# Kernel optimization log

Hardware: AMD Instinct MI355X
Metric: run time of the kernel (lower is better)

## Reference

```python
import jax, jax.numpy as jnp
import numpy as np

# dims: M=512 new tokens, N=2048 model dim, D=128 head dim, H=16 heads,
# L=4096 cache length, P=2048 cache write offset

def setup_inputs() -> dict:
    key = jax.random.key(0)
    k0, k1, k2, k3 = jax.random.split(key, 4)
    M, N, D, L = 512, 2048, 128, 4096
    X = jax.random.normal(k0, (M, N), jnp.float32)
    # scale weights ~1/sqrt(N) so projections have unit-ish scale
    W_qkv = jax.random.normal(k1, (N, 3 * N), jnp.float32) * (N ** -0.5)
    H = N // D
    cache_K = jax.random.normal(k2, (H, L, D), jnp.float32)
    # realistic cache state: keys stored in cache are RMS-normalized
    cache_K = cache_K * jax.lax.rsqrt(jnp.mean(cache_K * cache_K, axis=-1, keepdims=True))
    cache_V = jax.random.normal(k3, (H, L, D), jnp.float32)
    return {"X": X, "W_qkv": W_qkv, "cache_K": cache_K, "cache_V": cache_V, "P": 2048}


def reference(X, W_qkv, cache_K, cache_V, P):
    M = X.shape[0]
    H, L, D = cache_K.shape
    qkv = X @ W_qkv                              # [M, 3N]
    q, k, v = jnp.split(qkv, 3, axis=-1)         # each [M, N]
    q = q.reshape(M, H, D).transpose(1, 0, 2)    # [H, M, D]
    k = k.reshape(M, H, D).transpose(1, 0, 2)
    v = v.reshape(M, H, D).transpose(1, 0, 2)
    # RMS-style normalization (no learned gain, no eps in original)
    q = q * jax.lax.rsqrt(jnp.mean(q * q, axis=-1, keepdims=True))
    k = k * jax.lax.rsqrt(jnp.mean(k * k, axis=-1, keepdims=True))
    # scatter-update into KV cache at position P
    Kc = jax.lax.dynamic_update_slice(cache_K, k, (0, P, 0))  # [H, L, D]
    Vc = jax.lax.dynamic_update_slice(cache_V, v, (0, P, 0))
    # unmasked, unscaled attention over the full cache (faithful to original:
    # plain exp/sum, no max-subtraction, no 1/sqrt(D))
    scores = jnp.einsum('hmd,hld->hml', q, Kc)   # [H, M, L]
    w = jnp.exp(scores)
    w = w / jnp.sum(w, axis=-1, keepdims=True)
    out = jnp.einsum('hml,hld->hmd', w, Vc)      # [H, M, D]
    return out.transpose(1, 0, 2).reshape(M, H * D)
```

## Files before the change

kernel.cpp:

```cpp
#include <hip/hip_runtime.h>
#include <math.h>

typedef _Float16 half_t;
typedef _Float16 half8 __attribute__((ext_vector_type(8)));
typedef _Float16 half4_t __attribute__((ext_vector_type(4)));
typedef _Float16 half2_t __attribute__((ext_vector_type(2)));
typedef float floatx4 __attribute__((ext_vector_type(4)));

#define M_TOK 512
#define N_DIM 2048
#define D_HEAD 128
#define H_HEADS 16
#define L_CACHE 4096
#define THREE_N 6144
#define NCHUNK 8
#define LCHUNK 512

__global__ __launch_bounds__(256) void prep_kernel(const float* __restrict__ W,
                                                   const float* __restrict__ X,
                                                   half_t* __restrict__ W16T,
                                                   half_t* __restrict__ X16) {
    __shared__ half_t tile[64 * 66];
    int b = blockIdx.x;
    int t = threadIdx.x;

    if (b < 3072) {
        int n0 = (b % 96) * 64, k0 = (b / 96) * 64;
        {
            int k = t >> 2, c0 = (t & 3) * 16;
            const float* src = W + (size_t)(k0 + k) * THREE_N + n0 + c0;
            float4 v[4];
#pragma unroll
            for (int j = 0; j < 4; ++j) v[j] = *(const float4*)(src + j * 4);
#pragma unroll
            for (int j = 0; j < 4; ++j) {
                tile[(c0 + j * 4 + 0) * 66 + k] = (half_t)v[j].x;
                tile[(c0 + j * 4 + 1) * 66 + k] = (half_t)v[j].y;
                tile[(c0 + j * 4 + 2) * 66 + k] = (half_t)v[j].z;
                tile[(c0 + j * 4 + 3) * 66 + k] = (half_t)v[j].w;
            }
        }
        __syncthreads();
        {
            int n = t >> 2, kg = (t & 3) * 16;
            half_t* dst = W16T + (size_t)(n0 + n) * N_DIM + k0 + kg;
            *(half8*)(dst) = *(half8*)&tile[n * 66 + kg];
            *(half8*)(dst + 8) = *(half8*)&tile[n * 66 + kg + 8];
        }
        return;
    }
    b -= 3072;
    {
        size_t i = (size_t)b * 2048 + t * 4;
        float4 v0 = *(const float4*)(X + i);
        float4 v1 = *(const float4*)(X + i + 1024);
        half4_t h0 = {(half_t)v0.x, (half_t)v0.y, (half_t)v0.z, (half_t)v0.w};
        half4_t h1 = {(half_t)v1.x, (half_t)v1.y, (half_t)v1.z, (half_t)v1.w};
        *(half4_t*)(X16 + i) = h0;
        *(half4_t*)(X16 + i + 1024) = h1;
    }
}

__global__ __launch_bounds__(256, 5) void mega_kernel(const half_t* __restrict__ X16,
                                                      const half_t* __restrict__ W16T,
                                                      const float* __restrict__ cK,
                                                      const float* __restrict__ cV,
                                                      const int* __restrict__ Pp,
                                                      half_t* __restrict__ Q16,
                                                      half_t* __restrict__ K16,
                                                      half_t* __restrict__ V16T) {
    __shared__ __align__(16) char smem[25088];
    const int t = threadIdx.x;
    int b = blockIdx.x;

    if (b >= 384) {
        b -= 384;
        const int P = *Pp;
        if (b < 1024) {
            int h = b >> 6, l0 = (b & 63) * 64;
            if (l0 >= P && l0 + 64 <= P + M_TOK) return;
            size_t base = ((size_t)h * L_CACHE + l0) * D_HEAD;
            float4 v[8];
#pragma unroll
            for (int i = 0; i < 8; ++i)
                v[i] = *(const float4*)(cK + base + i * 1024 + t * 4);
#pragma unroll
            for (int i = 0; i < 8; ++i) {
                int row = l0 + ((i * 1024 + t * 4) >> 7);
                half4_t hh = {(half_t)v[i].x, (half_t)v[i].y, (half_t)v[i].z, (half_t)v[i].w};
                if (row < P || row >= P + M_TOK)
                    *(half4_t*)(K16 + base + i * 1024 + t * 4) = hh;
            }
            return;
        }
        b -= 1024;
        {
            int h = b >> 7;
            int rem = b & 127;
            int lt = rem >> 1, dt = rem & 1;
            int l0 = lt * 64, d0 = dt * 64;
            if (l0 >= P && l0 + 64 <= P + M_TOK) return;
            bool overlap = (l0 < P + M_TOK) && (l0 + 64 > P);
            half_t* tile = (half_t*)smem;
            {
                int l = t >> 2, c0 = (t & 3) * 16;
                const float* src = cV + ((size_t)h * L_CACHE + l0 + l) * D_HEAD + d0 + c0;
                float4 v[4];
#pragma unroll
                for (int j = 0; j < 4; ++j) v[j] = *(const float4*)(src + j * 4);
#pragma unroll
                for (int j = 0; j < 4; ++j) {
                    tile[(c0 + j * 4 + 0) * 66 + l] = (half_t)v[j].x;
                    tile[(c0 + j * 4 + 1) * 66 + l] = (half_t)v[j].y;
                    tile[(c0 + j * 4 + 2) * 66 + l] = (half_t)v[j].z;
                    tile[(c0 + j * 4 + 3) * 66 + l] = (half_t)v[j].w;
                }
            }
            __syncthreads();
            {
                int d = t >> 2, lg = (t & 3) * 16;
                half_t* dst = V16T + ((size_t)h * D_HEAD + d0 + d) * L_CACHE + l0 + lg;
                if (!overlap) {
                    *(half8*)(dst) = *(half8*)&tile[d * 66 + lg];
                    *(half8*)(dst + 8) = *(half8*)&tile[d * 66 + lg + 8];
                } else {
#pragma unroll
                    for (int j = 0; j < 16; ++j) {
                        int l = l0 + lg + j;
                        if (l < P || l >= P + M_TOK) dst[j] = tile[d * 66 + lg + j];
                    }
                }
            }
            return;
        }
    }

    half_t* As = (half_t*)smem;
    half_t* Bs = (half_t*)(smem + 8192);
    half_t* Vt = (half_t*)smem;
    float* ssb = (float*)(smem + 24576);
    const int wid = t >> 6, lane = t & 63;
    const int quad = lane >> 4, ln = lane & 15;
    const int bx = b % 48, by = b / 48;
    const int m0 = by * 64, n0 = bx * 128;
    const int wm = (wid >> 1) * 32, wn = (wid & 1) * 64;

    floatx4 acc[2][4] = {};

    const int ar = t >> 3, ag = (t & 7) * 8;
    const int br = t >> 3, bg = (t & 7) * 8;
    const int rdk = (ln & 7) << 3;

    for (int k0 = 0; k0 < N_DIM; k0 += 64) {
        __syncthreads();
#pragma unroll
        for (int p = 0; p < 2; ++p) {
            int r = ar + p * 32;
            *(half8*)&As[r * 64 + (ag ^ ((r & 7) << 3))] =
                *(const half8*)(X16 + (size_t)(m0 + r) * N_DIM + k0 + ag);
        }
#pragma unroll
        for (int p = 0; p < 4; ++p) {
            int r = br + p * 32;
            *(half8*)&Bs[r * 64 + (bg ^ ((r & 7) << 3))] =
                *(const half8*)(W16T + (size_t)(n0 + r) * N_DIM + k0 + bg);
        }
        __syncthreads();
#pragma unroll
        for (int kt = 0; kt < 2; ++kt) {
            half8 a[2], bb[4];
#pragma unroll
            for (int i = 0; i < 2; ++i)
                a[i] = *(half8*)&As[(wm + i * 16 + ln) * 64 + ((kt * 32 + quad * 8) ^ rdk)];
#pragma unroll
            for (int j = 0; j < 4; ++j)
                bb[j] = *(half8*)&Bs[(wn + j * 16 + ln) * 64 + ((kt * 32 + quad * 8) ^ rdk)];
#pragma unroll
            for (int i = 0; i < 2; ++i)
#pragma unroll
                for (int j = 0; j < 4; ++j)
                    acc[i][j] = __builtin_amdgcn_mfma_f32_16x16x32_f16(a[i], bb[j], acc[i][j], 0, 0, 0);
        }
    }

    const int seg = bx >> 4, h = bx & 15;
    const int P = *Pp;

    if (seg < 2) {
        float ss[2][4], scale[2][4];
#pragma unroll
        for (int i = 0; i < 2; ++i)
#pragma unroll
            for (int r = 0; r < 4; ++r) {
                float s = 0.f;
#pragma unroll
                for (int j = 0; j < 4; ++j) s += acc[i][j][r] * acc[i][j][r];
#pragma unroll
                for (int msk = 1; msk < 16; msk <<= 1) s += __shfl_xor(s, msk, 64);
                ss[i][r] = s;
            }
        if (ln == 0) {
#pragma unroll
            for (int i = 0; i < 2; ++i)
#pragma unroll
                for (int r = 0; r < 4; ++r)
                    ssb[wid * 32 + i * 16 + quad * 4 + r] = ss[i][r];
        }
        __syncthreads();
#pragma unroll
        for (int i = 0; i < 2; ++i)
#pragma unroll
            for (int r = 0; r < 4; ++r)
                scale[i][r] =
                    rsqrtf((ss[i][r] + ssb[(wid ^ 1) * 32 + i * 16 + quad * 4 + r]) * (1.0f / 128.0f));
#pragma unroll
        for (int i = 0; i < 2; ++i) {
            int mbase = m0 + wm + i * 16 + quad * 4;
#pragma unroll
            for (int j = 0; j < 4; ++j) {
                int col = wn + j * 16 + ln;
#pragma unroll
                for (int r = 0; r < 4; ++r) {
                    int m = mbase + r;
                    half_t val = (half_t)(acc[i][j][r] * scale[i][r]);
                    if (seg == 0)
                        Q16[((size_t)h * M_TOK + m) * D_HEAD + col] = val;
                    else
                        K16[((size_t)h * L_CACHE + P + m) * D_HEAD + col] = val;
                }
            }
        }
    } else {
        __syncthreads();
#pragma unroll
        for (int i = 0; i < 2; ++i) {
            int mbase = wm + i * 16 + quad * 4;
#pragma unroll
            for (int j = 0; j < 4; ++j) {
                int d = wn + j * 16 + ln;
#pragma unroll
                for (int r = 0; r < 4; ++r)
                    Vt[d * 72 + mbase + r] = (half_t)acc[i][j][r];
            }
        }
        __syncthreads();
#pragma unroll
        for (int p = 0; p < 4; ++p) {
            int s = p * 256 + t;
            int d = s >> 3, sg = s & 7;
            *(half8*)(V16T + ((size_t)h * D_HEAD + d) * L_CACHE + P + m0 + sg * 8) =
                *(half8*)&Vt[d * 72 + sg * 8];
        }
    }
}

__global__ __launch_bounds__(256, 4) void attn_partial_kernel(const half_t* __restrict__ Q16,
                                                              const half_t* __restrict__ K16,
                                                              const half_t* __restrict__ V16T,
                                                              half_t* __restrict__ Opart,
                                                              float* __restrict__ mstat,
                                                              float* __restrict__ lstat) {
    __shared__ half_t Ks[64 * 128];
    __shared__ half_t Vs[128 * 64];
    __shared__ half_t Ps[4 * 16 * 64];
    const int t = threadIdx.x, w = t >> 6, lane = t & 63;
    const int quad = lane >> 4, ln = lane & 15;

    const int bid = blockIdx.x;
    const int xcd = bid & 7, slot = bid >> 3;
    const int pair = (xcd << 4) | (slot >> 3);
    const int h = pair & 15, c = pair >> 4, mi = slot & 7;
    const int mb = mi * 64;

    const half_t* Qh = Q16 + (size_t)h * M_TOK * D_HEAD;
    const half_t* Kh = K16 + (size_t)h * L_CACHE * D_HEAD;
    const half_t* Vh = V16T + (size_t)h * D_HEAD * L_CACHE;

    const int m0 = mb + w * 16;
    half8 qf[4];
#pragma unroll
    for (int dt = 0; dt < 4; ++dt)
        qf[dt] = *(const half8*)(Qh + (size_t)(m0 + ln) * D_HEAD + dt * 32 + quad * 8);

    floatx4 oacc[8] = {};
    float mrow = -INFINITY;
    float lrow = 0.f;

    half_t* Pw = Ps + w * (16 * 64);
    const int psw = (ln & 7) << 3;

    const int l0base = c * LCHUNK;
    const int kr = t >> 4, kc = (t & 15) * 8;
    const int vr = t >> 3, vc = (t & 7) * 8;
    const int ksw = (kr & 7) << 3;
    const int vsw = (vr & 7) << 3;

    half8 kreg[4], vreg[4];
#pragma unroll
    for (int p = 0; p < 4; ++p) {
        kreg[p] = *(const half8*)(Kh + (size_t)(l0base + p * 16 + kr) * D_HEAD + kc);
        vreg[p] = *(const half8*)(Vh + (size_t)(p * 32 + vr) * L_CACHE + l0base + vc);
    }

    for (int it = 0; it < LCHUNK / 64; ++it) {
        __syncthreads();
#pragma unroll
        for (int p = 0; p < 4; ++p)
            *(half8*)&Ks[(p * 16 + kr) * 128 + (kc ^ ksw)] = kreg[p];
#pragma unroll
        for (int p = 0; p < 4; ++p)
            *(half8*)&Vs[(p * 32 + vr) * 64 + (vc ^ vsw)] = vreg[p];
        if (it + 1 < LCHUNK / 64) {
            int l1 = l0base + (it + 1) * 64;
#pragma unroll
            for (int p = 0; p < 4; ++p) {
                kreg[p] = *(const half8*)(Kh + (size_t)(l1 + p * 16 + kr) * D_HEAD + kc);
                vreg[p] = *(const half8*)(Vh + (size_t)(p * 32 + vr) * L_CACHE + l1 + vc);
            }
        }
        __syncthreads();

        floatx4 sacc[4] = {};
#pragma unroll
        for (int dt = 0; dt < 4; ++dt) {
            half8 kf[4];
#pragma unroll
            for (int nt = 0; nt < 4; ++nt)
                kf[nt] = *(half8*)&Ks[(nt * 16 + ln) * 128 + ((dt * 32 + quad * 8) ^ psw)];
#pragma unroll
            for (int nt = 0; nt < 4; ++nt)
                sacc[nt] = __builtin_amdgcn_mfma_f32_16x16x32_f16(kf[nt], qf[dt], sacc[nt], 0, 0, 0);
        }

        {
            float mx = sacc[0][0];
#pragma unroll
            for (int nt = 0; nt < 4; ++nt)
#pragma unroll
                for (int r = 0; r < 4; ++r) mx = fmaxf(mx, sacc[nt][r]);
            mx = fmaxf(mx, __shfl_xor(mx, 16));
            mx = fmaxf(mx, __shfl_xor(mx, 32));
            if (__ballot(mx > mrow)) {
                float mnew = fmaxf(mrow, mx);
                float alpha = __expf(mrow - mnew);
                mrow = mnew;
                lrow *= alpha;
                float ar[4];
#pragma unroll
                for (int r = 0; r < 4; ++r) ar[r] = __shfl(alpha, quad * 4 + r, 16);
#pragma unroll
                for (int nt8 = 0; nt8 < 8; ++nt8)
#pragma unroll
                    for (int r = 0; r < 4; ++r) oacc[nt8][r] *= ar[r];
            }
            float psum = 0.f;
#pragma unroll
            for (int nt = 0; nt < 4; ++nt) {
                half4_t h4;
#pragma unroll
                for (int r = 0; r < 4; ++r) {
                    float p = __expf(sacc[nt][r] - mrow);
                    psum += p;
                    h4[r] = (half_t)p;
                }
                *(half4_t*)&Pw[ln * 64 + ((nt * 16 + quad * 4) ^ psw)] = h4;
            }
            psum += __shfl_xor(psum, 16);
            psum += __shfl_xor(psum, 32);
            lrow += psum;
        }

#pragma unroll
        for (int kt = 0; kt < 2; ++kt) {
            half8 a = *(half8*)&Pw[ln * 64 + ((kt * 32 + quad * 8) ^ psw)];
#pragma unroll
            for (int nt8 = 0; nt8 < 8; ++nt8) {
                half8 b = *(half8*)&Vs[(nt8 * 16 + ln) * 64 + ((kt * 32 + quad * 8) ^ psw)];
                oacc[nt8] = __builtin_amdgcn_mfma_f32_16x16x32_f16(a, b, oacc[nt8], 0, 0, 0);
            }
        }
    }

    half_t* Oc = Opart + ((size_t)(c * H_HEADS + h) * M_TOK) * D_HEAD;
    float* ms = mstat + (size_t)(c * H_HEADS + h) * M_TOK;
    float* ls = lstat + (size_t)(c * H_HEADS + h) * M_TOK;
#pragma unroll
    for (int nt8 = 0; nt8 < 8; ++nt8) {
        int col = nt8 * 16 + ln;
#pragma unroll
        for (int r = 0; r < 4; ++r)
            Oc[(size_t)(m0 + quad * 4 + r) * D_HEAD + col] = (half_t)oacc[nt8][r];
    }
    if (lane < 16) {
        ms[m0 + lane] = mrow;
        ls[m0 + lane] = lrow;
    }
}

__global__ __launch_bounds__(256) void combine_kernel(const half_t* __restrict__ Opart,
                                                      const float* __restrict__ mstat,
                                                      const float* __restrict__ lstat,
                                                      float* __restrict__ out) {
    int gw = blockIdx.x * 4 + (threadIdx.x >> 6);
    int lane = threadIdx.x & 63;
    int h = gw >> 9, m = gw & 511;
    int d = lane * 2;

    float ms[NCHUNK];
    float mg = -INFINITY;
#pragma unroll
    for (int c = 0; c < NCHUNK; ++c) {
        ms[c] = mstat[((c * H_HEADS + h) << 9) + m];
        mg = fmaxf(mg, ms[c]);
    }
    float denom = 0.f, o0 = 0.f, o1 = 0.f;
#pragma unroll
    for (int c = 0; c < NCHUNK; ++c) {
        float e = __expf(ms[c] - mg);
        denom += lstat[((c * H_HEADS + h) << 9) + m] * e;
        const half_t* Oc = Opart + (((size_t)(c * H_HEADS + h) << 9) + m) * D_HEAD + d;
        half2_t v = *(const half2_t*)Oc;
        o0 += (float)v.x * e;
        o1 += (float)v.y * e;
    }
    float inv = 1.0f / denom;
    float* op = out + (size_t)m * N_DIM + h * D_HEAD + d;
    op[0] = o0 * inv;
    op[1] = o1 * inv;
}

extern "C" void kernel_launch(void* const* d_in, const int* in_sizes, int n_in,
                              void* d_out, int out_size, void* d_ws, size_t ws_size,
                              hipStream_t stream) {
    const float* X = (const float*)d_in[0];
    const float* W = (const float*)d_in[1];
    const float* cK = (const float*)d_in[2];
    const float* cV = (const float*)d_in[3];
    const int* Pp = (const int*)d_in[4];
    float* out = (float*)d_out;

    char* ws = (char*)d_ws;
    half_t* Q16 = (half_t*)(ws + 0);
    half_t* K16 = (half_t*)(ws + 2097152);
    half_t* V16T = (half_t*)(ws + 18874368);
    half_t* X16 = (half_t*)(ws + 35651584);
    half_t* W16T = (half_t*)(ws + 37748736);
    half_t* Opart = (half_t*)(ws + 37748736);
    float* mstat = (float*)(ws + 71303168);
    float* lstat = (float*)(ws + 71827456);

    prep_kernel<<<3584, 256, 0, stream>>>(W, X, W16T, X16);
    mega_kernel<<<3456, 256, 0, stream>>>(X16, W16T, cK, cV, Pp, Q16, K16, V16T);
    attn_partial_kernel<<<1024, 256, 0, stream>>>(Q16, K16, V16T, Opart, mstat, lstat);
    combine_kernel<<<2048, 256, 0, stream>>>(Opart, mstat, lstat, out);
}
```

Before: 214.4 us.

## Fuse K cache fp16 conversion into attention loads, drop separate K16 pass

Removes the mega_kernel blocks that convert the fp32 K cache to an fp16 K16 buffer. The attention kernel now reads fp32 cache_K directly, converting on the fly, and reads newly projected keys from a compact Knew buffer when the row falls in the P window. This saves a full write and re-read of the fp16 K cache, but the attention kernel's K loads double in bytes (fp32) and gain a per-row branch.

Measured after the change: 253.2 us. +18.1%, slower.

```diff
diff --git a/kernel.cpp b/kernel.cpp
--- a/kernel.cpp
+++ b/kernel.cpp
@@ -63,11 +63,10 @@
 
 __global__ __launch_bounds__(256, 5) void mega_kernel(const half_t* __restrict__ X16,
                                                       const half_t* __restrict__ W16T,
-                                                      const float* __restrict__ cK,
                                                       const float* __restrict__ cV,
                                                       const int* __restrict__ Pp,
                                                       half_t* __restrict__ Q16,
-                                                      half_t* __restrict__ K16,
+                                                      half_t* __restrict__ Knew,
                                                       half_t* __restrict__ V16T) {
     __shared__ __align__(16) char smem[25088];
     const int t = threadIdx.x;
@@ -76,24 +75,6 @@
     if (b >= 384) {
         b -= 384;
         const int P = *Pp;
-        if (b < 1024) {
-            int h = b >> 6, l0 = (b & 63) * 64;
-            if (l0 >= P && l0 + 64 <= P + M_TOK) return;
-            size_t base = ((size_t)h * L_CACHE + l0) * D_HEAD;
-            float4 v[8];
-#pragma unroll
-            for (int i = 0; i < 8; ++i)
-                v[i] = *(const float4*)(cK + base + i * 1024 + t * 4);
-#pragma unroll
-            for (int i = 0; i < 8; ++i) {
-                int row = l0 + ((i * 1024 + t * 4) >> 7);
-                half4_t hh = {(half_t)v[i].x, (half_t)v[i].y, (half_t)v[i].z, (half_t)v[i].w};
-                if (row < P || row >= P + M_TOK)
-                    *(half4_t*)(K16 + base + i * 1024 + t * 4) = hh;
-            }
-            return;
-        }
-        b -= 1024;
         {
             int h = b >> 7;
             int rem = b & 127;
@@ -226,7 +207,7 @@
                     if (seg == 0)
                         Q16[((size_t)h * M_TOK + m) * D_HEAD + col] = val;
                     else
-                        K16[((size_t)h * L_CACHE + P + m) * D_HEAD + col] = val;
+                        Knew[((size_t)h * M_TOK + m) * D_HEAD + col] = val;
                 }
             }
         }
@@ -255,8 +236,10 @@
 }
 
 __global__ __launch_bounds__(256, 4) void attn_partial_kernel(const half_t* __restrict__ Q16,
-                                                              const half_t* __restrict__ K16,
+                                                              const float* __restrict__ cK,
+                                                              const half_t* __restrict__ Knew,
                                                               const half_t* __restrict__ V16T,
+                                                              const int* __restrict__ Pp,
                                                               half_t* __restrict__ Opart,
                                                               float* __restrict__ mstat,
                                                               float* __restrict__ lstat) {
@@ -271,9 +254,11 @@
     const int pair = (xcd << 4) | (slot >> 3);
     const int h = pair & 15, c = pair >> 4, mi = slot & 7;
     const int mb = mi * 64;
+    const int P = *Pp;
 
     const half_t* Qh = Q16 + (size_t)h * M_TOK * D_HEAD;
-    const half_t* Kh = K16 + (size_t)h * L_CACHE * D_HEAD;
+    const float* Kh32 = cK + (size_t)h * L_CACHE * D_HEAD;
+    const half_t* Khn = Knew + (size_t)h * M_TOK * D_HEAD;
     const half_t* Vh = V16T + (size_t)h * D_HEAD * L_CACHE;
 
     const int m0 = mb + w * 16;
@@ -295,10 +280,23 @@
     const int ksw = (kr & 7) << 3;
     const int vsw = (vr & 7) << 3;
 
+    auto loadK = [&](int l) -> half8 {
+        if (l >= P && l < P + M_TOK) {
+            return *(const half8*)(Khn + (size_t)(l - P) * D_HEAD + kc);
+        } else {
+            const float* s = Kh32 + (size_t)l * D_HEAD + kc;
+            float4 u0 = *(const float4*)s;
+            float4 u1 = *(const float4*)(s + 4);
+            half8 r = {(half_t)u0.x, (half_t)u0.y, (half_t)u0.z, (half_t)u0.w,
+                       (half_t)u1.x, (half_t)u1.y, (half_t)u1.z, (half_t)u1.w};
+            return r;
+        }
+    };
+
     half8 kreg[4], vreg[4];
 #pragma unroll
     for (int p = 0; p < 4; ++p) {
-        kreg[p] = *(const half8*)(Kh + (size_t)(l0base + p * 16 + kr) * D_HEAD + kc);
+        kreg[p] = loadK(l0base + p * 16 + kr);
         vreg[p] = *(const half8*)(Vh + (size_t)(p * 32 + vr) * L_CACHE + l0base + vc);
     }
 
@@ -314,7 +312,7 @@
             int l1 = l0base + (it + 1) * 64;
 #pragma unroll
             for (int p = 0; p < 4; ++p) {
-                kreg[p] = *(const half8*)(Kh + (size_t)(l1 + p * 16 + kr) * D_HEAD + kc);
+                kreg[p] = loadK(l1 + p * 16 + kr);
                 vreg[p] = *(const half8*)(Vh + (size_t)(p * 32 + vr) * L_CACHE + l1 + vc);
             }
         }
@@ -441,7 +439,7 @@
 
     char* ws = (char*)d_ws;
     half_t* Q16 = (half_t*)(ws + 0);
-    half_t* K16 = (half_t*)(ws + 2097152);
+    half_t* Knew = (half_t*)(ws + 2097152);
     half_t* V16T = (half_t*)(ws + 18874368);
     half_t* X16 = (half_t*)(ws + 35651584);
     half_t* W16T = (half_t*)(ws + 37748736);
@@ -450,7 +448,7 @@
     float* lstat = (float*)(ws + 71827456);
 
     prep_kernel<<<3584, 256, 0, stream>>>(W, X, W16T, X16);
-    mega_kernel<<<3456, 256, 0, stream>>>(X16, W16T, cK, cV, Pp, Q16, K16, V16T);
-    attn_partial_kernel<<<1024, 256, 0, stream>>>(Q16, K16, V16T, Opart, mstat, lstat);
+    mega_kernel<<<2432, 256, 0, stream>>>(X16, W16T, cV, Pp, Q16, Knew, V16T);
+    attn_partial_kernel<<<1024, 256, 0, stream>>>(Q16, cK, Knew, V16T, Pp, Opart, mstat, lstat);
     combine_kernel<<<2048, 256, 0, stream>>>(Opart, mstat, lstat, out);
 }
```
